# Performance work log

Hardware: AMD Instinct MI355X
Metric: run time of the kernel (lower is better)

Reference implementation:

```python
import jax, jax.numpy as jnp
import numpy as np

N = 8192        # nodes
D_IN = 256      # in_dims
D_OUT = 32      # out_dims (assignment clusters)


def setup_inputs() -> dict:
    key = jax.random.key(0)
    k1, k2, k3 = jax.random.split(key, 3)
    main_feat = jax.random.normal(k1, (N, D_IN), dtype=jnp.float32)
    main_adj = jax.random.uniform(k2, (N, N), dtype=jnp.float32)
    W = jax.random.normal(k3, (D_IN, D_OUT), dtype=jnp.float32) * (1.0 / np.sqrt(D_IN))
    b = jnp.zeros((D_OUT,), dtype=jnp.float32)
    return {"main_feat": main_feat, "main_adj": main_adj, "W": W, "b": b}


def reference(main_feat, main_adj, W, b):
    # GraphConvolution: support = X @ W ; out = A @ support + b   -> [N, D_OUT]
    support = main_feat @ W
    assign = main_adj @ support + b
    # softmax over the NODE axis (dim 0), matching F.softmax(main_assign, 0)
    assign = jax.nn.softmax(assign, axis=0)
    # pooling: raw_emb = assign^T @ X  -> [D_OUT, D_IN]
    raw_emb = assign.T @ main_feat
    return raw_emb
```

## Files before the change

### kernel.cpp

```cpp
#include <hip/hip_runtime.h>
#include <stdint.h>

#define NN   8192
#define DIN  256
#define DOUT 32

#define PPART (NN * DOUT + 320)
#define PP4   (DOUT * DIN + 320)

typedef short bf16x8 __attribute__((ext_vector_type(8)));
typedef float f32x16 __attribute__((ext_vector_type(16)));

union BF8 { uint32_t u[4]; bf16x8 v; };

__device__ __forceinline__ void split_pair(float a, float b, uint32_t& hp, uint32_t& lp) {
    uint32_t ua = __float_as_uint(a), ub = __float_as_uint(b);
    hp = (ua >> 16) | (ub & 0xffff0000u);
    float la = a - __uint_as_float(ua & 0xffff0000u);
    float lb = b - __uint_as_float(ub & 0xffff0000u);
    lp = (__float_as_uint(la) >> 16) | (__float_as_uint(lb) & 0xffff0000u);
}

__global__ __launch_bounds__(256) void k1_support(
    const float* __restrict__ X, const float* __restrict__ W,
    unsigned short* __restrict__ hi_frag, unsigned short* __restrict__ lo_frag)
{
    __shared__ float Xs[32 * 256];
    int t = threadIdx.x;
    int kbase = blockIdx.x * 32;

    const float4* Xg = (const float4*)(X + (size_t)kbase * DIN);
    float4* Xs4 = (float4*)Xs;
#pragma unroll
    for (int p = 0; p < 8; ++p) Xs4[p * 256 + t] = Xg[p * 256 + t];
    __syncthreads();

    int c = t & 31;
    int q = t >> 5;
    int kb2  = q >> 2;
    int half = (q >> 1) & 1;
    int j4   = q & 1;
    int krow0 = kb2 * 16 + half * 8 + j4 * 4;

    float acc[4] = {0.f, 0.f, 0.f, 0.f};
    for (int d = 0; d < 256; ++d) {
        float w = W[d * 32 + c];
#pragma unroll
        for (int jj = 0; jj < 4; ++jj)
            acc[jj] += Xs[(krow0 + jj) * 256 + d] * w;
    }

    uint32_t h01, l01, h23, l23;
    split_pair(acc[0], acc[1], h01, l01);
    split_pair(acc[2], acc[3], h23, l23);

    int ks = (kbase >> 4) + kb2;
    size_t elembase = (size_t)ks * 512 + (size_t)(half * 32 + c) * 8 + j4 * 4;
    *(uint2*)(hi_frag + elembase) = make_uint2(h01, h23);
    *(uint2*)(lo_frag + elembase) = make_uint2(l01, l23);
}

__global__ __launch_bounds__(512) void k2_logits(
    const float* __restrict__ adj,
    const unsigned short* __restrict__ hi_frag,
    const unsigned short* __restrict__ lo_frag,
    float* __restrict__ part)
{
    __shared__ __align__(16) float tile[32 * 260];
    int t = threadIdx.x;
    int lane = t & 63, wv = t >> 6;
    int row0 = blockIdx.x * 32;
    size_t col0 = (size_t)blockIdx.y * 2048;

    f32x16 acc;
#pragma unroll
    for (int i = 0; i < 16; ++i) acc[i] = 0.f;

    int r  = lane & 31;
    int hs = lane >> 5;
    int tl0 = blockIdx.x & 7;

    const float* asrc = adj + (size_t)(row0 + wv) * NN + col0 + lane * 4;

    float4 pref[4];
    {
#pragma unroll
        for (int p = 0; p < 4; ++p)
            pref[p] = *(const float4*)(asrc + (size_t)(8 * p) * NN + tl0 * 256);
#pragma unroll
        for (int p = 0; p < 4; ++p)
            *(float4*)((char*)tile + (wv + 8 * p) * 1040 + lane * 16) = pref[p];
    }

    for (int tt = 0; tt < 8; ++tt) {
        int tl  = (tt + tl0) & 7;
        int tln = (tt + 1 + tl0) & 7;
        if (tt < 7) {
#pragma unroll
            for (int p = 0; p < 4; ++p)
                pref[p] = *(const float4*)(asrc + (size_t)(8 * p) * NN + tln * 256);
        }
        __syncthreads();
#pragma unroll
        for (int ss = 0; ss < 2; ++ss) {
            int s = 2 * wv + ss;
            const float4* ap = (const float4*)((const char*)tile + r * 1040 + s * 64 + hs * 32);
            float4 a0 = ap[0];
            float4 a1 = ap[1];
            int ks = (int)blockIdx.y * 128 + tl * 16 + s;
            BF8 bh, bl, ah, al;
            bh.v = *(const bf16x8*)(hi_frag + (size_t)ks * 512 + lane * 8);
            bl.v = *(const bf16x8*)(lo_frag + (size_t)ks * 512 + lane * 8);
            split_pair(a0.x, a0.y, ah.u[0], al.u[0]);
            split_pair(a0.z, a0.w, ah.u[1], al.u[1]);
            split_pair(a1.x, a1.y, ah.u[2], al.u[2]);
            split_pair(a1.z, a1.w, ah.u[3], al.u[3]);
            acc = __builtin_amdgcn_mfma_f32_32x32x16_bf16(ah.v, bh.v, acc, 0, 0, 0);
            acc = __builtin_amdgcn_mfma_f32_32x32x16_bf16(ah.v, bl.v, acc, 0, 0, 0);
            acc = __builtin_amdgcn_mfma_f32_32x32x16_bf16(al.v, bh.v, acc, 0, 0, 0);
        }
        if (tt < 7) {
            __syncthreads();
#pragma unroll
            for (int p = 0; p < 4; ++p)
                *(float4*)((char*)tile + (wv + 8 * p) * 1040 + lane * 16) = pref[p];
        }
    }

    __syncthreads();
    float* red = tile;
#pragma unroll
    for (int g = 0; g < 16; ++g) red[wv * 1024 + lane * 16 + g] = acc[g];
    __syncthreads();

    float* pdst = part + (size_t)blockIdx.y * PPART + (size_t)row0 * 32;
    for (int a = t; a < 1024; a += 512) {
        int row = a >> 5, colc = a & 31;
        int l = colc + 32 * ((row >> 2) & 1);
        int g = (row & 3) | ((row >> 3) << 2);
        float ssum = 0.f;
#pragma unroll
        for (int w8 = 0; w8 < 8; ++w8) ssum += red[w8 * 1024 + l * 16 + g];
        pdst[a] = ssum;
    }
}

__global__ __launch_bounds__(256) void k3a_sum_max(
    const float* __restrict__ part, float* __restrict__ logits_sum,
    float* __restrict__ Mpart)
{
    __shared__ float red[256 * 4];
    int t = threadIdx.x;
    size_t f = (size_t)blockIdx.x * 256 + t;

    float4 v = make_float4(0.f, 0.f, 0.f, 0.f);
#pragma unroll
    for (int pp = 0; pp < 4; ++pp) {
        int p = (pp + blockIdx.x) & 3;
        float4 u = ((const float4*)(part + (size_t)p * PPART))[f];
        v.x += u.x; v.y += u.y; v.z += u.z; v.w += u.w;
    }
    ((float4*)logits_sum)[f] = v;

    red[t * 4 + 0] = v.x; red[t * 4 + 1] = v.y;
    red[t * 4 + 2] = v.z; red[t * 4 + 3] = v.w;
    __syncthreads();
    for (int s = 128; s >= 8; s >>= 1) {
        if (t < s)
#pragma unroll
            for (int j = 0; j < 4; ++j)
                red[t * 4 + j] = fmaxf(red[t * 4 + j], red[(t + s) * 4 + j]);
        __syncthreads();
    }
    if (t < 8)
#pragma unroll
        for (int j = 0; j < 4; ++j)
            Mpart[blockIdx.x * 32 + t * 4 + j] = red[t * 4 + j];
}

__global__ __launch_bounds__(256) void k3b_exp_sum(
    const float* __restrict__ logits_sum, const float* __restrict__ Mpart,
    float* __restrict__ e_buf, float* __restrict__ Spart)
{
    __shared__ float red[256 * 4];
    int t = threadIdx.x;
    int c = t & 31, g0 = t >> 5;

    float m = -3.4e38f;
#pragma unroll
    for (int gg = 0; gg < 32; ++gg)
        m = fmaxf(m, Mpart[(g0 * 32 + gg) * 32 + c]);
    red[t] = m;
    __syncthreads();
    for (int s = 128; s >= 32; s >>= 1) {
        if (t < s) red[t] = fmaxf(red[t], red[t + s]);
        __syncthreads();
    }
    float m0 = red[(4 * t + 0) & 31], m1 = red[(4 * t + 1) & 31];
    float m2 = red[(4 * t + 2) & 31], m3 = red[(4 * t + 3) & 31];
    __syncthreads();

    size_t f = (size_t)blockIdx.x * 256 + t;
    float4 v = ((const float4*)logits_sum)[f];
    v.x = __expf(v.x - m0); v.y = __expf(v.y - m1);
    v.z = __expf(v.z - m2); v.w = __expf(v.w - m3);
    ((float4*)e_buf)[f] = v;

    red[t * 4 + 0] = v.x; red[t * 4 + 1] = v.y;
    red[t * 4 + 2] = v.z; red[t * 4 + 3] = v.w;
    __syncthreads();
    for (int s = 128; s >= 8; s >>= 1) {
        if (t < s)
#pragma unroll
            for (int j = 0; j < 4; ++j)
                red[t * 4 + j] += red[(t + s) * 4 + j];
        __syncthreads();
    }
    if (t < 8)
#pragma unroll
        for (int j = 0; j < 4; ++j)
            Spart[blockIdx.x * 32 + t * 4 + j] = red[t * 4 + j];
}

__global__ __launch_bounds__(256) void k4_pool(
    const float* __restrict__ X, const float* __restrict__ e_buf,
    float* __restrict__ p4)
{
    __shared__ float Xs[8 * 256];
    __shared__ float As[8 * 32];
    int t = threadIdx.x;
    int c = t & 31, dg = t >> 5;
    int ibase = blockIdx.x * 32;

    float acc[32];
#pragma unroll
    for (int i = 0; i < 32; ++i) acc[i] = 0.f;

    for (int rnd = 0; rnd < 4; ++rnd) {
        __syncthreads();
        const float4* Xg = (const float4*)(X + (size_t)(ibase + rnd * 8) * DIN);
        float4* Xs4 = (float4*)Xs;
        Xs4[t]       = Xg[t];
        Xs4[256 + t] = Xg[256 + t];
        As[t] = e_buf[(size_t)(ibase + rnd * 8 + (t >> 5)) * 32 + (t & 31)];
        __syncthreads();
#pragma unroll
        for (int i2 = 0; i2 < 8; ++i2) {
            float a = As[i2 * 32 + c];
#pragma unroll
            for (int dd = 0; dd < 32; ++dd)
                acc[dd] += a * Xs[i2 * 256 + dg * 32 + dd];
        }
    }
    float* dst = p4 + (size_t)blockIdx.x * PP4 + (size_t)c * 256 + dg * 32;
#pragma unroll
    for (int v = 0; v < 8; ++v)
        ((float4*)dst)[v] = make_float4(acc[v * 4], acc[v * 4 + 1], acc[v * 4 + 2], acc[v * 4 + 3]);
}

__global__ __launch_bounds__(256) void k5_reduce(
    const float* __restrict__ p4, const float* __restrict__ Spart,
    float* __restrict__ out)
{
    __shared__ float red[256];
    __shared__ float sred[256];
    int t = threadIdx.x;
    int c_out = blockIdx.x >> 3;

    sred[t] = Spart[t * 32 + c_out];

    int j = blockIdx.x * 32 + (t & 31);
    int g0 = t >> 5;
    float a = 0.f;
#pragma unroll
    for (int gg = 0; gg < 32; ++gg) {
        int g = (g0 * 32 + gg + blockIdx.x) & 255;
        a += p4[(size_t)g * PP4 + j];
    }
    red[t] = a;
    __syncthreads();
    for (int s = 128; s >= 32; s >>= 1) {
        if (t < s) { red[t] += red[t + s]; sred[t] += sred[t + s]; }
        __syncthreads();
    }
    if (t < 32) {
        float sv = sred[t];
#pragma unroll
        for (int off = 16; off >= 1; off >>= 1) sv += __shfl_xor(sv, off);
        out[blockIdx.x * 32 + t] = red[t] / sv;
    }
}

extern "C" void kernel_launch(void* const* d_in, const int* in_sizes, int n_in,
                              void* d_out, int out_size, void* d_ws, size_t ws_size,
                              hipStream_t stream) {
    const float* X   = (const float*)d_in[0];
    const float* adj = (const float*)d_in[1];
    const float* W   = (const float*)d_in[2];
    float* out = (float*)d_out;

    char* w = (char*)d_ws;
    unsigned short* hi_frag = (unsigned short*)w;
    unsigned short* lo_frag = (unsigned short*)(w + 512 * 1024);
    size_t off = 1024 * 1024;
    float* part = (float*)(w + off);            off += (size_t)4 * PPART * sizeof(float);
    float* logits_sum = (float*)(w + off);      off += (size_t)NN * DOUT * sizeof(float);
    float* e_buf = (float*)(w + off);           off += (size_t)NN * DOUT * sizeof(float);
    float* Mpart = (float*)(w + off);           off += 256 * 32 * sizeof(float);
    float* Spart = (float*)(w + off);           off += 256 * 32 * sizeof(float);
    float* p4 = (float*)(w + off);              off += (size_t)256 * PP4 * sizeof(float);

    k1_support<<<NN / 32, 256, 0, stream>>>(X, W, hi_frag, lo_frag);
    k2_logits<<<dim3(NN / 32, 4), 512, 0, stream>>>(adj, hi_frag, lo_frag, part);
    k3a_sum_max<<<256, 256, 0, stream>>>(part, logits_sum, Mpart);
    k3b_exp_sum<<<256, 256, 0, stream>>>(logits_sum, Mpart, e_buf, Spart);
    k4_pool<<<256, 256, 0, stream>>>(X, e_buf, p4);
    k5_reduce<<<256, 256, 0, stream>>>(p4, Spart, out);
}
```

Baseline: 448.9 us.

## Fuse softmax and pooling tail kernels into one persistent kernel with grid barriers

Merges the four tail kernels (sum/max, exp/sum, pool, reduce) into one 256-block kernel that uses atomic-counter grid barriers between phases. Logits and exponentials stay in registers and shared memory instead of round-tripping through global buffers. This removes three kernel launches and the logits_sum and e_buf traffic. In exchange it relies on all 256 blocks being co-resident for the spin barrier, and on k1 resetting the barrier counters each call.

New measurement: 491.4 us. 9.5% more time.

```diff
diff --git a/kernel.cpp b/kernel.cpp
--- a/kernel.cpp
+++ b/kernel.cpp
@@ -7,6 +7,7 @@
 
 #define PPART (NN * DOUT + 320)
 #define PP4   (DOUT * DIN + 320)
+#define NBLK_T 256
 
 typedef short bf16x8 __attribute__((ext_vector_type(8)));
 typedef float f32x16 __attribute__((ext_vector_type(16)));
@@ -21,13 +22,27 @@
     lp = (__float_as_uint(la) >> 16) | (__float_as_uint(lb) & 0xffff0000u);
 }
 
+__device__ __forceinline__ void grid_barrier(int* bar) {
+    __syncthreads();
+    if (threadIdx.x == 0) {
+        __threadfence();
+        __hip_atomic_fetch_add(bar, 1, __ATOMIC_RELAXED, __HIP_MEMORY_SCOPE_AGENT);
+        while (__hip_atomic_load(bar, __ATOMIC_RELAXED, __HIP_MEMORY_SCOPE_AGENT) < NBLK_T) {}
+        __threadfence();
+    }
+    __syncthreads();
+}
+
 __global__ __launch_bounds__(256) void k1_support(
     const float* __restrict__ X, const float* __restrict__ W,
-    unsigned short* __restrict__ hi_frag, unsigned short* __restrict__ lo_frag)
+    unsigned short* __restrict__ hi_frag, unsigned short* __restrict__ lo_frag,
+    int* __restrict__ bars)
 {
     __shared__ float Xs[32 * 256];
     int t = threadIdx.x;
     int kbase = blockIdx.x * 32;
+
+    if (blockIdx.x == 0 && t < 2) bars[t] = 0;
 
     const float4* Xg = (const float4*)(X + (size_t)kbase * DIN);
     float4* Xs4 = (float4*)Xs;
@@ -145,23 +160,26 @@
     }
 }
 
-__global__ __launch_bounds__(256) void k3a_sum_max(
-    const float* __restrict__ part, float* __restrict__ logits_sum,
-    float* __restrict__ Mpart)
+__global__ __launch_bounds__(256) void kt_tail(
+    const float* __restrict__ part, const float* __restrict__ X,
+    float* __restrict__ Mpart, float* __restrict__ Spart,
+    float* __restrict__ p4, float* __restrict__ out, int* __restrict__ bars)
 {
     __shared__ float red[256 * 4];
+    __shared__ float As[32 * 32];
+    __shared__ float Xs[8 * 256];
+    __shared__ float sred[256];
     int t = threadIdx.x;
-    size_t f = (size_t)blockIdx.x * 256 + t;
-
+    int b = blockIdx.x;
+
+    size_t f = (size_t)b * 256 + t;
     float4 v = make_float4(0.f, 0.f, 0.f, 0.f);
 #pragma unroll
     for (int pp = 0; pp < 4; ++pp) {
-        int p = (pp + blockIdx.x) & 3;
+        int p = (pp + b) & 3;
         float4 u = ((const float4*)(part + (size_t)p * PPART))[f];
         v.x += u.x; v.y += u.y; v.z += u.z; v.w += u.w;
     }
-    ((float4*)logits_sum)[f] = v;
-
     red[t * 4 + 0] = v.x; red[t * 4 + 1] = v.y;
     red[t * 4 + 2] = v.z; red[t * 4 + 3] = v.w;
     __syncthreads();
@@ -175,22 +193,18 @@
     if (t < 8)
 #pragma unroll
         for (int j = 0; j < 4; ++j)
-            Mpart[blockIdx.x * 32 + t * 4 + j] = red[t * 4 + j];
-}
-
-__global__ __launch_bounds__(256) void k3b_exp_sum(
-    const float* __restrict__ logits_sum, const float* __restrict__ Mpart,
-    float* __restrict__ e_buf, float* __restrict__ Spart)
-{
-    __shared__ float red[256 * 4];
-    int t = threadIdx.x;
+            Mpart[b * 32 + t * 4 + j] = red[t * 4 + j];
+
+    grid_barrier(bars + 0);
+
     int c = t & 31, g0 = t >> 5;
-
-    float m = -3.4e38f;
-#pragma unroll
-    for (int gg = 0; gg < 32; ++gg)
-        m = fmaxf(m, Mpart[(g0 * 32 + gg) * 32 + c]);
-    red[t] = m;
+    {
+        float m = -3.4e38f;
+#pragma unroll
+        for (int gg = 0; gg < 32; ++gg)
+            m = fmaxf(m, Mpart[(g0 * 32 + gg) * 32 + c]);
+        red[t] = m;
+    }
     __syncthreads();
     for (int s = 128; s >= 32; s >>= 1) {
         if (t < s) red[t] = fmaxf(red[t], red[t + s]);
@@ -200,12 +214,15 @@
     float m2 = red[(4 * t + 2) & 31], m3 = red[(4 * t + 3) & 31];
     __syncthreads();
 
-    size_t f = (size_t)blockIdx.x * 256 + t;
-    float4 v = ((const float4*)logits_sum)[f];
     v.x = __expf(v.x - m0); v.y = __expf(v.y - m1);
     v.z = __expf(v.z - m2); v.w = __expf(v.w - m3);
-    ((float4*)e_buf)[f] = v;
-
+    {
+        int row = t >> 3, cb = (4 * t) & 31;
+        As[row * 32 + cb]     = v.x;
+        As[row * 32 + cb + 1] = v.y;
+        As[row * 32 + cb + 2] = v.z;
+        As[row * 32 + cb + 3] = v.w;
+    }
     red[t * 4 + 0] = v.x; red[t * 4 + 1] = v.y;
     red[t * 4 + 2] = v.z; red[t * 4 + 3] = v.w;
     __syncthreads();
@@ -219,19 +236,10 @@
     if (t < 8)
 #pragma unroll
         for (int j = 0; j < 4; ++j)
-            Spart[blockIdx.x * 32 + t * 4 + j] = red[t * 4 + j];
-}
-
-__global__ __launch_bounds__(256) void k4_pool(
-    const float* __restrict__ X, const float* __restrict__ e_buf,
-    float* __restrict__ p4)
-{
-    __shared__ float Xs[8 * 256];
-    __shared__ float As[8 * 32];
-    int t = threadIdx.x;
-    int c = t & 31, dg = t >> 5;
-    int ibase = blockIdx.x * 32;
-
+            Spart[b * 32 + t * 4 + j] = red[t * 4 + j];
+
+    int dg = t >> 5;
+    int ibase = b * 32;
     float acc[32];
 #pragma unroll
     for (int i = 0; i < 32; ++i) acc[i] = 0.f;
@@ -242,39 +250,33 @@
         float4* Xs4 = (float4*)Xs;
         Xs4[t]       = Xg[t];
         Xs4[256 + t] = Xg[256 + t];
-        As[t] = e_buf[(size_t)(ibase + rnd * 8 + (t >> 5)) * 32 + (t & 31)];
         __syncthreads();
 #pragma unroll
         for (int i2 = 0; i2 < 8; ++i2) {
-            float a = As[i2 * 32 + c];
+            float a = As[(rnd * 8 + i2) * 32 + c];
 #pragma unroll
             for (int dd = 0; dd < 32; ++dd)
                 acc[dd] += a * Xs[i2 * 256 + dg * 32 + dd];
         }
     }
-    float* dst = p4 + (size_t)blockIdx.x * PP4 + (size_t)c * 256 + dg * 32;
-#pragma unroll
-    for (int v = 0; v < 8; ++v)
-        ((float4*)dst)[v] = make_float4(acc[v * 4], acc[v * 4 + 1], acc[v * 4 + 2], acc[v * 4 + 3]);
-}
-
-__global__ __launch_bounds__(256) void k5_reduce(
-    const float* __restrict__ p4, const float* __restrict__ Spart,
-    float* __restrict__ out)
-{
-    __shared__ float red[256];
-    __shared__ float sred[256];
-    int t = threadIdx.x;
-    int c_out = blockIdx.x >> 3;
-
+    {
+        float* dst = p4 + (size_t)b * PP4 + (size_t)c * 256 + dg * 32;
+#pragma unroll
+        for (int q = 0; q < 8; ++q)
+            ((float4*)dst)[q] = make_float4(acc[q * 4], acc[q * 4 + 1],
+                                            acc[q * 4 + 2], acc[q * 4 + 3]);
+    }
+
+    grid_barrier(bars + 1);
+
+    int c_out = b >> 3;
     sred[t] = Spart[t * 32 + c_out];
 
-    int j = blockIdx.x * 32 + (t & 31);
-    int g0 = t >> 5;
+    int j = b * 32 + (t & 31);
     float a = 0.f;
 #pragma unroll
     for (int gg = 0; gg < 32; ++gg) {
-        int g = (g0 * 32 + gg + blockIdx.x) & 255;
+        int g = (g0 * 32 + gg + b) & 255;
         a += p4[(size_t)g * PP4 + j];
     }
     red[t] = a;
@@ -287,7 +289,7 @@
         float sv = sred[t];
 #pragma unroll
         for (int off = 16; off >= 1; off >>= 1) sv += __shfl_xor(sv, off);
-        out[blockIdx.x * 32 + t] = red[t] / sv;
+        out[b * 32 + t] = red[t] / sv;
     }
 }
 
@@ -303,17 +305,14 @@
     unsigned short* hi_frag = (unsigned short*)w;
     unsigned short* lo_frag = (unsigned short*)(w + 512 * 1024);
     size_t off = 1024 * 1024;
-    float* part = (float*)(w + off);            off += (size_t)4 * PPART * sizeof(float);
-    float* logits_sum = (float*)(w + off);      off += (size_t)NN * DOUT * sizeof(float);
-    float* e_buf = (float*)(w + off);           off += (size_t)NN * DOUT * sizeof(float);
-    float* Mpart = (float*)(w + off);           off += 256 * 32 * sizeof(float);
-    float* Spart = (float*)(w + off);           off += 256 * 32 * sizeof(float);
-    float* p4 = (float*)(w + off);              off += (size_t)256 * PP4 * sizeof(float);
-
-    k1_support<<<NN / 32, 256, 0, stream>>>(X, W, hi_frag, lo_frag);
+    float* part = (float*)(w + off);   off += (size_t)4 * PPART * sizeof(float);
+    float* Mpart = (float*)(w + off);  off += 256 * 32 * sizeof(float);
+    float* Spart = (float*)(w + off);  off += 256 * 32 * sizeof(float);
+    float* p4 = (float*)(w + off);     off += (size_t)256 * PP4 * sizeof(float);
+    off = (off + 127) & ~(size_t)127;
+    int* bars = (int*)(w + off);       off += 128;
+
+    k1_support<<<NN / 32, 256, 0, stream>>>(X, W, hi_frag, lo_frag, bars);
     k2_logits<<<dim3(NN / 32, 4), 512, 0, stream>>>(adj, hi_frag, lo_frag, part);
-    k3a_sum_max<<<256, 256, 0, stream>>>(part, logits_sum, Mpart);
-    k3b_exp_sum<<<256, 256, 0, stream>>>(logits_sum, Mpart, e_buf, Spart);
-    k4_pool<<<256, 256, 0, stream>>>(X, e_buf, p4);
-    k5_reduce<<<256, 256, 0, stream>>>(p4, Spart, out);
-}
+    kt_tail<<<NBLK_T, 256, 0, stream>>>(part, X, Mpart, Spart, p4, out, bars);
+}
```
